# Kernel tuning notes

Measured on AMD Instinct MI355X. Metric: run time of the kernel, lower is better.

The kernel has to match this reference:

```python
import jax, jax.numpy as jnp
import numpy as np

K = 128      # knowledge_n (= net1 = prednet output width)
LOW = 64     # low_dim
PP = 64      # pp_dim
STU = 50000  # student_n
EXER = 20000 # exer_n
S_RANGES = [(0, 9999), (10000, 19999)]
NR = len(S_RANGES)
B = 4096


def setup_inputs() -> dict:
    key = jax.random.key(0)
    ks = jax.random.split(key, 16)

    def xavier(k, shape):
        fan_in, fan_out = shape[-1], shape[-2] if len(shape) > 1 else shape[-1]
        lim = np.sqrt(6.0 / (fan_in + fan_out))
        return jax.random.uniform(k, shape, jnp.float32, -lim, lim)

    return {
        "stu_id": jax.random.randint(ks[0], (B,), 0, STU),
        "exer_id": jax.random.randint(ks[1], (B,), 0, EXER),
        "kn_emb": jnp.ones((B, K), jnp.float32),
        "student_emb": xavier(ks[2], (NR, STU, LOW)),          # ParameterList stacked
        "prompt_stu": xavier(ks[3], (STU, PP)),
        "knowledge_emb": jax.random.normal(ks[4], (K, LOW), jnp.float32),
        "k_difficulty": xavier(ks[5], (EXER, LOW)),
        "s_exer_vectors": jax.random.uniform(ks[6], (NR, PP), jnp.float32),
        "W1": xavier(ks[7], (K, K + LOW)),                      # prednet_full1 (no bias)
        "W2": xavier(ks[8], (K, K + LOW)),                      # prednet_full2 (no bias)
        "W3": xavier(ks[9], (1, K)),                            # prednet_full3
        "b3": jnp.zeros((1,), jnp.float32),
        "fc1_W": xavier(ks[10], (K, PP + K)),
        "fc1_b": jnp.zeros((K,), jnp.float32),
        "fc2_W": xavier(ks[11], (K, PP + K)),
        "fc2_b": jnp.zeros((K,), jnp.float32),
    }


def reference(stu_id, exer_id, kn_emb, student_emb, prompt_stu, knowledge_emb,
              k_difficulty, s_exer_vectors, W1, W2, W3, b3, fc1_W, fc1_b, fc2_W, fc2_b):
    sig = jax.nn.sigmoid
    kle = knowledge_emb  # [K, LOW]

    # --- student side ---
    # prompt_stu.repeat(NR, 1) then index_select == index prompt_stu with stu_id % STU
    p_stu = prompt_stu[stu_id % STU]                              # [B, PP]
    stu_cat = student_emb.reshape(NR * STU, LOW)                  # concat of ParameterList
    old_stu = sig(stu_cat[stu_id] @ kle.T)                        # [B, K]
    stu_e = sig(jnp.concatenate([p_stu, old_stu], 1) @ fc1_W.T + fc1_b)  # [B, K]

    # --- exercise side ---
    counts = np.array([r[1] - r[0] + 1 for r in S_RANGES])
    temp_vectors = jnp.repeat(s_exer_vectors, counts, axis=0, total_repeat_length=EXER)
    p_exer = sig(temp_vectors[exer_id])                           # [B, PP]
    old_exer = sig(sig(k_difficulty[exer_id]) @ kle.T)            # [B, K]
    exer_e = sig(jnp.concatenate([p_exer, old_exer], 1) @ fc2_W.T + fc2_b)  # [B, K]

    # --- per-concept interaction ---
    # cat([x_broadcast, kn_vector], 2) @ W.T splits into x @ Wa.T + kle @ Wb.T
    W1a, W1b = W1[:, :K], W1[:, K:]
    W2a, W2b = W2[:, :K], W2[:, K:]
    preference = sig((stu_e @ W1a.T)[:, None, :] + (kle @ W1b.T)[None, :, :])   # [B, K, K]
    diff = sig((exer_e @ W2a.T)[:, None, :] + (kle @ W2b.T)[None, :, :])        # [B, K, K]

    o = sig((preference - diff) @ W3.T + b3)                      # [B, K, 1]
    sum_out = jnp.sum(o * kn_emb[:, :, None], axis=1)             # [B, 1]
    count = jnp.sum(kn_emb, axis=1, keepdims=True)
    return sum_out / count
```

## Files before the change

kernel.cpp:

```cpp
#include <hip/hip_runtime.h>
#include <hip/hip_bf16.h>

#define STUN   50000
#define BATCH  4096
#define LOG2E  1.4426950408889634f

__device__ __forceinline__ float fexp2(float x){ return __builtin_amdgcn_exp2f(x); }
__device__ __forceinline__ float frcp (float x){ return __builtin_amdgcn_rcpf(x); }
__device__ __forceinline__ float fsig (float x){ return frcp(1.0f + fexp2(-LOG2E * x)); }

__global__ __launch_bounds__(128) void k_pre(
    const float* __restrict__ kle,
    const float* __restrict__ W1,
    const float* __restrict__ W2,
    const float* __restrict__ fc1_W,
    const float* __restrict__ fc2_W,
    float* __restrict__ kleT,
    float* __restrict__ fc1T,
    float* __restrict__ fc2T,
    float* __restrict__ W1aT,
    float* __restrict__ W2aT,
    float* __restrict__ E1i,
    float* __restrict__ E2i)
{
    const int bid = blockIdx.x;
    const int t   = threadIdx.x;
    if (bid < 64) {
        const int u = bid;
        kleT[u * 128 + t] = kle[t * 64 + u];
    } else if (bid < 256) {
        const int u = bid - 64;
        fc1T[u * 128 + t] = fc1_W[t * 192 + u];
    } else if (bid < 448) {
        const int u = bid - 256;
        fc2T[u * 128 + t] = fc2_W[t * 192 + u];
    } else if (bid < 576) {
        const int u = bid - 448;
        W1aT[u * 128 + t] = W1[t * 192 + u];
    } else if (bid < 704) {
        const int u = bid - 576;
        W2aT[u * 128 + t] = W2[t * 192 + u];
    } else if (bid < 832) {
        const int j = bid - 704;
        float acc = 0.f;
        #pragma unroll
        for (int u4 = 0; u4 < 16; ++u4) {
            const float4 kv = *(const float4*)&kle[t * 64 + u4 * 4];
            const float4 wv = *(const float4*)&W1[j * 192 + 128 + u4 * 4];
            acc += kv.x * wv.x + kv.y * wv.y + kv.z * wv.z + kv.w * wv.w;
        }
        E1i[((j >> 2) * 128 + t) * 4 + (j & 3)] = fexp2(-LOG2E * acc);
    } else {
        const int j = bid - 832;
        float acc = 0.f;
        #pragma unroll
        for (int u4 = 0; u4 < 16; ++u4) {
            const float4 kv = *(const float4*)&kle[t * 64 + u4 * 4];
            const float4 wv = *(const float4*)&W2[j * 192 + 128 + u4 * 4];
            acc += kv.x * wv.x + kv.y * wv.y + kv.z * wv.z + kv.w * wv.w;
        }
        E2i[((j >> 2) * 128 + t) * 4 + (j & 3)] = fexp2(-LOG2E * acc);
    }
}

__global__ __launch_bounds__(256, 2) void k_prep(
    const int*   __restrict__ stu_id,
    const int*   __restrict__ exer_id,
    const float* __restrict__ student_emb,
    const float* __restrict__ prompt_stu,
    const float* __restrict__ k_diff,
    const float* __restrict__ s_exer,
    const float* __restrict__ kleT,
    const float* __restrict__ fc1T,
    const float* __restrict__ fc2T,
    const float* __restrict__ W1aT,
    const float* __restrict__ W2aT,
    const float* __restrict__ fc1_b,
    const float* __restrict__ fc2_b,
    float* __restrict__ es1o,
    float* __restrict__ es2o)
{
    __shared__ __align__(16) float sh_in [4][64][8];
    __shared__ __align__(16) float sh_old[2][128][12];
    __shared__ __align__(16) float sh_e  [2][128][12];
    __shared__ __align__(16) float ps[4][2][32][36];

    const int t  = threadIdx.x;
    const int b0 = blockIdx.x * 8;

    {
        const int g   = t >> 5;
        const int l   = t & 31;
        const int sid = stu_id[b0 + g];
        const int eid = exer_id[b0 + g];
        const int er  = (eid >= 10000) ? 1 : 0;
        #pragma unroll
        for (int it = 0; it < 2; ++it) {
            const int u = l + 32 * it;
            sh_in[0][u][g] = student_emb[sid * 64 + u];
            sh_in[1][u][g] = fsig(k_diff[eid * 64 + u]);
            sh_in[2][u][g] = prompt_stu[(sid % STUN) * 64 + u];
            sh_in[3][u][g] = fsig(s_exer[er * 64 + u]);
        }
    }
    __syncthreads();

    const int wv   = t >> 6;
    const int l    = t & 63;
    const int half = l >> 5;
    const int iq   = l & 31;
    float* myps = &ps[wv][half][iq][0];

    const int ch   = t >> 7;
    const int cidx = t & 127;
    const int ciq  = cidx >> 2;
    const int cc   = cidx & 3;

    float a[4][8];

#define CLR { _Pragma("unroll") for (int c = 0; c < 4; ++c) \
              _Pragma("unroll") for (int b = 0; b < 8; ++b) a[c][b] = 0.f; }

#define FMAC(c, wc) { \
    a[c][0] = fmaf(wc, x0.x, a[c][0]); a[c][1] = fmaf(wc, x0.y, a[c][1]); \
    a[c][2] = fmaf(wc, x0.z, a[c][2]); a[c][3] = fmaf(wc, x0.w, a[c][3]); \
    a[c][4] = fmaf(wc, x1.x, a[c][4]); a[c][5] = fmaf(wc, x1.y, a[c][5]); \
    a[c][6] = fmaf(wc, x1.z, a[c][6]); a[c][7] = fmaf(wc, x1.w, a[c][7]); }

#define GSTEP(wp, xp) { \
    const float4 w4 = *(const float4*)(wp); \
    const float4 x0 = *(const float4*)&(xp)[0]; \
    const float4 x1 = *(const float4*)&(xp)[4]; \
    FMAC(0, w4.x); FMAC(1, w4.y); FMAC(2, w4.z); FMAC(3, w4.w); }

#define PSTORE { _Pragma("unroll") for (int b = 0; b < 8; ++b) \
    *(float4*)&myps[b * 4] = make_float4(a[0][b], a[1][b], a[2][b], a[3][b]); }

#define PCOMB(res) float res[8]; \
    _Pragma("unroll") for (int b = 0; b < 8; ++b) \
        res[b] = ps[0][ch][ciq][b * 4 + cc] + ps[1][ch][ciq][b * 4 + cc] \
               + ps[2][ch][ciq][b * 4 + cc] + ps[3][ch][ciq][b * 4 + cc];

    CLR;
    {
        const int u0 = wv * 16;
        #pragma unroll 4
        for (int u = u0; u < u0 + 16; ++u)
            GSTEP(&kleT[u * 128 + iq * 4], sh_in[half][u]);
    }
    PSTORE;
    __syncthreads();
    {
        PCOMB(s);
        #pragma unroll
        for (int b = 0; b < 8; ++b) sh_old[ch][cidx][b] = fsig(s[b]);
    }
    __syncthreads();

    CLR;
    {
        const float* fcT = half ? fc2T : fc1T;
        const int u0 = wv * 48;
        const int ue_in = (u0 + 48 < 64) ? u0 + 48 : 64;
        #pragma unroll 4
        for (int u = u0; u < ue_in; ++u)
            GSTEP(&fcT[u * 128 + iq * 4], sh_in[2 + half][u]);
        const int us_old = (u0 > 64) ? u0 : 64;
        #pragma unroll 4
        for (int u = us_old; u < u0 + 48; ++u)
            GSTEP(&fcT[u * 128 + iq * 4], sh_old[half][u - 64]);
    }
    PSTORE;
    __syncthreads();
    {
        PCOMB(s);
        const float bias = (ch ? fc2_b : fc1_b)[cidx];
        #pragma unroll
        for (int b = 0; b < 8; ++b) sh_e[ch][cidx][b] = fsig(s[b] + bias);
    }
    __syncthreads();

    CLR;
    {
        const float* WT = half ? W2aT : W1aT;
        const int u0 = wv * 32;
        #pragma unroll 4
        for (int u = u0; u < u0 + 32; ++u)
            GSTEP(&WT[u * 128 + iq * 4], sh_e[half][u]);
    }
    PSTORE;
    __syncthreads();
    {
        PCOMB(s);
        float* eso = ch ? es2o : es1o;
        #pragma unroll
        for (int b = 0; b < 8; ++b)
            eso[(b0 + b) * 128 + cidx] = fexp2(-LOG2E * s[b]);
    }
#undef CLR
#undef FMAC
#undef GSTEP
#undef PSTORE
#undef PCOMB
}

__global__ __launch_bounds__(256, 6) void k_main(
    const float* __restrict__ es1o,
    const float* __restrict__ es2o,
    const float* __restrict__ E1i,
    const float* __restrict__ E2i,
    const float* __restrict__ W3,
    const float* __restrict__ b3,
    const float* __restrict__ kn,
    float* __restrict__ out)
{
    __shared__ __align__(16) float ses[2][2][128];
    __shared__ float sW3[128];
    __shared__ __align__(16) float redj[2][64][2];
    __shared__ float red2_o[2][2];
    __shared__ float red2_k[2][2];

    const int t   = threadIdx.x;
    const int b0  = blockIdx.x * 2;

    if (t < 128) {
        const int row  = t >> 5;
        const int col4 = (t & 31) * 4;
        const float* src = (row < 2) ? es1o : es2o;
        *(float4*)&ses[row >> 1][row & 1][col4] =
            *(const float4*)&src[(b0 + (row & 1)) * 128 + col4];
    } else if (t < 160) {
        const int q = t - 128;
        *(float4*)&sW3[q * 4] = *(const float4*)&W3[q * 4];
    }
    __syncthreads();

    const int w   = t >> 6;
    const int kk  = t & 63;
    const int kh  = w & 1;
    const int jh  = w >> 1;
    const int k2  = kh * 64 + kk;

    const float4* E1v = (const float4*)E1i;
    const float4* E2v = (const float4*)E2i;

    float acc0 = 0.f, acc1 = 0.f;

#define COMP(acc, esv1, esv2, e1c, e2c, w3c) { \
        const float uu = (esv1) * (e1c); \
        const float vv = (esv2) * (e2c); \
        const float dd = frcp((1.f + uu) * (1.f + vv)); \
        acc += ((vv - uu) * dd) * (w3c); }

    #pragma unroll 4
    for (int j4 = 0; j4 < 16; ++j4) {
        const int jj4 = jh * 16 + j4;
        const int j   = jj4 * 4;
        const float4 e1  = E1v[jj4 * 128 + k2];
        const float4 e2  = E2v[jj4 * 128 + k2];
        const float4 w3  = *(const float4*)&sW3[j];
        const float4 s1a = *(const float4*)&ses[0][0][j];
        const float4 s1b = *(const float4*)&ses[0][1][j];
        const float4 s2a = *(const float4*)&ses[1][0][j];
        const float4 s2b = *(const float4*)&ses[1][1][j];

        COMP(acc0, s1a.x, s2a.x, e1.x, e2.x, w3.x);
        COMP(acc0, s1a.y, s2a.y, e1.y, e2.y, w3.y);
        COMP(acc0, s1a.z, s2a.z, e1.z, e2.z, w3.z);
        COMP(acc0, s1a.w, s2a.w, e1.w, e2.w, w3.w);
        COMP(acc1, s1b.x, s2b.x, e1.x, e2.x, w3.x);
        COMP(acc1, s1b.y, s2b.y, e1.y, e2.y, w3.y);
        COMP(acc1, s1b.z, s2b.z, e1.z, e2.z, w3.z);
        COMP(acc1, s1b.w, s2b.w, e1.w, e2.w, w3.w);
    }
#undef COMP

    if (jh == 1) {
        redj[kh][kk][0] = acc0;
        redj[kh][kk][1] = acc1;
    }
    __syncthreads();
    if (jh == 0) {
        const float bb3 = b3[0];
        const float t0 = acc0 + redj[kh][kk][0];
        const float t1 = acc1 + redj[kh][kk][1];
        const float o0 = fsig(t0 + bb3);
        const float o1 = fsig(t1 + bb3);
        const float kn0 = kn[(b0 + 0) * 128 + k2];
        const float kn1 = kn[(b0 + 1) * 128 + k2];
        float co0 = o0 * kn0, ck0 = kn0;
        float co1 = o1 * kn1, ck1 = kn1;
        #pragma unroll
        for (int off = 1; off < 64; off <<= 1) {
            co0 += __shfl_xor(co0, off);
            ck0 += __shfl_xor(ck0, off);
            co1 += __shfl_xor(co1, off);
            ck1 += __shfl_xor(ck1, off);
        }
        if (kk == 0) {
            red2_o[kh][0] = co0; red2_o[kh][1] = co1;
            red2_k[kh][0] = ck0; red2_k[kh][1] = ck1;
        }
    }
    __syncthreads();
    if (t < 2) {
        const float so = red2_o[0][t] + red2_o[1][t];
        const float sk = red2_k[0][t] + red2_k[1][t];
        out[b0 + t] = so / sk;
    }
}

extern "C" void kernel_launch(void* const* d_in, const int* in_sizes, int n_in,
                              void* d_out, int out_size, void* d_ws, size_t ws_size,
                              hipStream_t stream)
{
    const int*   stu_id      = (const int*)  d_in[0];
    const int*   exer_id     = (const int*)  d_in[1];
    const float* kn_emb      = (const float*)d_in[2];
    const float* student_emb = (const float*)d_in[3];
    const float* prompt_stu  = (const float*)d_in[4];
    const float* kle         = (const float*)d_in[5];
    const float* k_diff      = (const float*)d_in[6];
    const float* s_exer      = (const float*)d_in[7];
    const float* W1          = (const float*)d_in[8];
    const float* W2          = (const float*)d_in[9];
    const float* W3          = (const float*)d_in[10];
    const float* b3          = (const float*)d_in[11];
    const float* fc1_W       = (const float*)d_in[12];
    const float* fc1_b       = (const float*)d_in[13];
    const float* fc2_W       = (const float*)d_in[14];
    const float* fc2_b       = (const float*)d_in[15];
    float* out = (float*)d_out;

    float* ws   = (float*)d_ws;
    float* kleT = ws;
    float* fc1T = kleT + 8192;
    float* fc2T = fc1T + 24576;
    float* W1aT = fc2T + 24576;
    float* W2aT = W1aT + 16384;
    float* E1i  = W2aT + 16384;
    float* E2i  = E1i  + 16384;
    float* es1o = E2i  + 16384;
    float* es2o = es1o + BATCH * 128;

    k_pre <<<960, 128, 0, stream>>>(kle, W1, W2, fc1_W, fc2_W,
                                    kleT, fc1T, fc2T, W1aT, W2aT, E1i, E2i);
    k_prep<<<BATCH / 8, 256, 0, stream>>>(stu_id, exer_id, student_emb, prompt_stu,
                                          k_diff, s_exer, kleT, fc1T, fc2T,
                                          W1aT, W2aT, fc1_b, fc2_b, es1o, es2o);
    k_main<<<BATCH / 2, 256, 0, stream>>>(es1o, es2o, E1i, E2i, W3, b3, kn_emb, out);
}
```

Baseline: 48.03 us.

## Fuse per-sample prep and pairwise interaction kernels into one launch

Merges k_prep and k_main into a single kernel that processes 4 samples per block. The per-sample es1/es2 exponentials stay in shared memory instead of round-tripping through global memory, and one kernel launch is removed. Each block now also walks all 128 j values per k, so the cross-wave j reduction goes away. The cost is halving the batch per block in the GEMM phase, which means more reloads of the weight matrices per sample, and the pairwise phase loses the 2-way j split.

```diff
diff --git a/kernel.cpp b/kernel.cpp
--- a/kernel.cpp
+++ b/kernel.cpp
@@ -63,7 +63,7 @@
     }
 }
 
-__global__ __launch_bounds__(256, 2) void k_prep(
+__global__ __launch_bounds__(256, 4) void k_fused(
     const int*   __restrict__ stu_id,
     const int*   __restrict__ exer_id,
     const float* __restrict__ student_emb,
@@ -77,31 +77,34 @@
     const float* __restrict__ W2aT,
     const float* __restrict__ fc1_b,
     const float* __restrict__ fc2_b,
-    float* __restrict__ es1o,
-    float* __restrict__ es2o)
+    const float* __restrict__ E1i,
+    const float* __restrict__ E2i,
+    const float* __restrict__ W3,
+    const float* __restrict__ b3,
+    const float* __restrict__ kn,
+    float* __restrict__ out)
 {
-    __shared__ __align__(16) float sh_in [4][64][8];
-    __shared__ __align__(16) float sh_old[2][128][12];
-    __shared__ __align__(16) float sh_e  [2][128][12];
-    __shared__ __align__(16) float ps[4][2][32][36];
+    __shared__ __align__(16) float sh_in [4][64][4];
+    __shared__ __align__(16) float sh_old[2][128][4];
+    __shared__ __align__(16) float sh_e  [2][128][4];
+    __shared__ __align__(16) float ps[4][2][32][20];
+    __shared__ __align__(16) float ses[2][4][128];
+    __shared__ float r_o[4][2];
+    __shared__ float r_k[4][2];
 
     const int t  = threadIdx.x;
-    const int b0 = blockIdx.x * 8;
-
-    {
-        const int g   = t >> 5;
-        const int l   = t & 31;
+    const int b0 = blockIdx.x * 4;
+
+    {
+        const int g   = t >> 6;
+        const int u   = t & 63;
         const int sid = stu_id[b0 + g];
         const int eid = exer_id[b0 + g];
         const int er  = (eid >= 10000) ? 1 : 0;
-        #pragma unroll
-        for (int it = 0; it < 2; ++it) {
-            const int u = l + 32 * it;
-            sh_in[0][u][g] = student_emb[sid * 64 + u];
-            sh_in[1][u][g] = fsig(k_diff[eid * 64 + u]);
-            sh_in[2][u][g] = prompt_stu[(sid % STUN) * 64 + u];
-            sh_in[3][u][g] = fsig(s_exer[er * 64 + u]);
-        }
+        sh_in[0][u][g] = student_emb[sid * 64 + u];
+        sh_in[1][u][g] = fsig(k_diff[eid * 64 + u]);
+        sh_in[2][u][g] = prompt_stu[(sid % STUN) * 64 + u];
+        sh_in[3][u][g] = fsig(s_exer[er * 64 + u]);
     }
     __syncthreads();
 
@@ -116,28 +119,25 @@
     const int ciq  = cidx >> 2;
     const int cc   = cidx & 3;
 
-    float a[4][8];
+    float a[4][4];
 
 #define CLR { _Pragma("unroll") for (int c = 0; c < 4; ++c) \
-              _Pragma("unroll") for (int b = 0; b < 8; ++b) a[c][b] = 0.f; }
+              _Pragma("unroll") for (int b = 0; b < 4; ++b) a[c][b] = 0.f; }
 
 #define FMAC(c, wc) { \
     a[c][0] = fmaf(wc, x0.x, a[c][0]); a[c][1] = fmaf(wc, x0.y, a[c][1]); \
-    a[c][2] = fmaf(wc, x0.z, a[c][2]); a[c][3] = fmaf(wc, x0.w, a[c][3]); \
-    a[c][4] = fmaf(wc, x1.x, a[c][4]); a[c][5] = fmaf(wc, x1.y, a[c][5]); \
-    a[c][6] = fmaf(wc, x1.z, a[c][6]); a[c][7] = fmaf(wc, x1.w, a[c][7]); }
+    a[c][2] = fmaf(wc, x0.z, a[c][2]); a[c][3] = fmaf(wc, x0.w, a[c][3]); }
 
 #define GSTEP(wp, xp) { \
     const float4 w4 = *(const float4*)(wp); \
     const float4 x0 = *(const float4*)&(xp)[0]; \
-    const float4 x1 = *(const float4*)&(xp)[4]; \
     FMAC(0, w4.x); FMAC(1, w4.y); FMAC(2, w4.z); FMAC(3, w4.w); }
 
-#define PSTORE { _Pragma("unroll") for (int b = 0; b < 8; ++b) \
+#define PSTORE { _Pragma("unroll") for (int b = 0; b < 4; ++b) \
     *(float4*)&myps[b * 4] = make_float4(a[0][b], a[1][b], a[2][b], a[3][b]); }
 
-#define PCOMB(res) float res[8]; \
-    _Pragma("unroll") for (int b = 0; b < 8; ++b) \
+#define PCOMB(res) float res[4]; \
+    _Pragma("unroll") for (int b = 0; b < 4; ++b) \
         res[b] = ps[0][ch][ciq][b * 4 + cc] + ps[1][ch][ciq][b * 4 + cc] \
                + ps[2][ch][ciq][b * 4 + cc] + ps[3][ch][ciq][b * 4 + cc];
 
@@ -153,7 +153,7 @@
     {
         PCOMB(s);
         #pragma unroll
-        for (int b = 0; b < 8; ++b) sh_old[ch][cidx][b] = fsig(s[b]);
+        for (int b = 0; b < 4; ++b) sh_old[ch][cidx][b] = fsig(s[b]);
     }
     __syncthreads();
 
@@ -176,7 +176,7 @@
         PCOMB(s);
         const float bias = (ch ? fc2_b : fc1_b)[cidx];
         #pragma unroll
-        for (int b = 0; b < 8; ++b) sh_e[ch][cidx][b] = fsig(s[b] + bias);
+        for (int b = 0; b < 4; ++b) sh_e[ch][cidx][b] = fsig(s[b] + bias);
     }
     __syncthreads();
 
@@ -192,57 +192,23 @@
     __syncthreads();
     {
         PCOMB(s);
-        float* eso = ch ? es2o : es1o;
-        #pragma unroll
-        for (int b = 0; b < 8; ++b)
-            eso[(b0 + b) * 128 + cidx] = fexp2(-LOG2E * s[b]);
+        #pragma unroll
+        for (int b = 0; b < 4; ++b)
+            ses[ch][b][cidx] = fexp2(-LOG2E * s[b]);
     }
 #undef CLR
 #undef FMAC
 #undef GSTEP
 #undef PSTORE
 #undef PCOMB
-}
-
-__global__ __launch_bounds__(256, 6) void k_main(
-    const float* __restrict__ es1o,
-    const float* __restrict__ es2o,
-    const float* __restrict__ E1i,
-    const float* __restrict__ E2i,
-    const float* __restrict__ W3,
-    const float* __restrict__ b3,
-    const float* __restrict__ kn,
-    float* __restrict__ out)
-{
-    __shared__ __align__(16) float ses[2][2][128];
-    __shared__ float sW3[128];
-    __shared__ __align__(16) float redj[2][64][2];
-    __shared__ float red2_o[2][2];
-    __shared__ float red2_k[2][2];
-
-    const int t   = threadIdx.x;
-    const int b0  = blockIdx.x * 2;
-
-    if (t < 128) {
-        const int row  = t >> 5;
-        const int col4 = (t & 31) * 4;
-        const float* src = (row < 2) ? es1o : es2o;
-        *(float4*)&ses[row >> 1][row & 1][col4] =
-            *(const float4*)&src[(b0 + (row & 1)) * 128 + col4];
-    } else if (t < 160) {
-        const int q = t - 128;
-        *(float4*)&sW3[q * 4] = *(const float4*)&W3[q * 4];
-    }
-    __syncthreads();
-
-    const int w   = t >> 6;
-    const int kk  = t & 63;
-    const int kh  = w & 1;
-    const int jh  = w >> 1;
-    const int k2  = kh * 64 + kk;
-
-    const float4* E1v = (const float4*)E1i;
-    const float4* E2v = (const float4*)E2i;
+    __syncthreads();
+
+    const int k  = t & 127;
+    const int bh = t >> 7;
+    const int i0 = bh * 2;
+
+    const float4* E1v = (const float4*)E1i + k;
+    const float4* E2v = (const float4*)E2i + k;
 
     float acc0 = 0.f, acc1 = 0.f;
 
@@ -250,63 +216,55 @@
         const float uu = (esv1) * (e1c); \
         const float vv = (esv2) * (e2c); \
         const float dd = frcp((1.f + uu) * (1.f + vv)); \
-        acc += ((vv - uu) * dd) * (w3c); }
+        acc = fmaf((vv - uu) * dd, (w3c), acc); }
 
     #pragma unroll 4
-    for (int j4 = 0; j4 < 16; ++j4) {
-        const int jj4 = jh * 16 + j4;
-        const int j   = jj4 * 4;
-        const float4 e1  = E1v[jj4 * 128 + k2];
-        const float4 e2  = E2v[jj4 * 128 + k2];
-        const float4 w3  = *(const float4*)&sW3[j];
-        const float4 s1a = *(const float4*)&ses[0][0][j];
-        const float4 s1b = *(const float4*)&ses[0][1][j];
-        const float4 s2a = *(const float4*)&ses[1][0][j];
-        const float4 s2b = *(const float4*)&ses[1][1][j];
-
-        COMP(acc0, s1a.x, s2a.x, e1.x, e2.x, w3.x);
-        COMP(acc0, s1a.y, s2a.y, e1.y, e2.y, w3.y);
-        COMP(acc0, s1a.z, s2a.z, e1.z, e2.z, w3.z);
-        COMP(acc0, s1a.w, s2a.w, e1.w, e2.w, w3.w);
-        COMP(acc1, s1b.x, s2b.x, e1.x, e2.x, w3.x);
-        COMP(acc1, s1b.y, s2b.y, e1.y, e2.y, w3.y);
-        COMP(acc1, s1b.z, s2b.z, e1.z, e2.z, w3.z);
-        COMP(acc1, s1b.w, s2b.w, e1.w, e2.w, w3.w);
+    for (int j4 = 0; j4 < 32; ++j4) {
+        const int j = j4 * 4;
+        const float4 e1  = E1v[j4 * 128];
+        const float4 e2  = E2v[j4 * 128];
+        const float4 w3  = *(const float4*)&W3[j];
+        const float4 p1a = *(const float4*)&ses[0][i0 + 0][j];
+        const float4 p2a = *(const float4*)&ses[1][i0 + 0][j];
+        const float4 p1b = *(const float4*)&ses[0][i0 + 1][j];
+        const float4 p2b = *(const float4*)&ses[1][i0 + 1][j];
+        COMP(acc0, p1a.x, p2a.x, e1.x, e2.x, w3.x);
+        COMP(acc0, p1a.y, p2a.y, e1.y, e2.y, w3.y);
+        COMP(acc0, p1a.z, p2a.z, e1.z, e2.z, w3.z);
+        COMP(acc0, p1a.w, p2a.w, e1.w, e2.w, w3.w);
+        COMP(acc1, p1b.x, p2b.x, e1.x, e2.x, w3.x);
+        COMP(acc1, p1b.y, p2b.y, e1.y, e2.y, w3.y);
+        COMP(acc1, p1b.z, p2b.z, e1.z, e2.z, w3.z);
+        COMP(acc1, p1b.w, p2b.w, e1.w, e2.w, w3.w);
     }
 #undef COMP
 
-    if (jh == 1) {
-        redj[kh][kk][0] = acc0;
-        redj[kh][kk][1] = acc1;
-    }
-    __syncthreads();
-    if (jh == 0) {
-        const float bb3 = b3[0];
-        const float t0 = acc0 + redj[kh][kk][0];
-        const float t1 = acc1 + redj[kh][kk][1];
-        const float o0 = fsig(t0 + bb3);
-        const float o1 = fsig(t1 + bb3);
-        const float kn0 = kn[(b0 + 0) * 128 + k2];
-        const float kn1 = kn[(b0 + 1) * 128 + k2];
-        float co0 = o0 * kn0, ck0 = kn0;
-        float co1 = o1 * kn1, ck1 = kn1;
-        #pragma unroll
-        for (int off = 1; off < 64; off <<= 1) {
-            co0 += __shfl_xor(co0, off);
-            ck0 += __shfl_xor(ck0, off);
-            co1 += __shfl_xor(co1, off);
-            ck1 += __shfl_xor(ck1, off);
-        }
-        if (kk == 0) {
-            red2_o[kh][0] = co0; red2_o[kh][1] = co1;
-            red2_k[kh][0] = ck0; red2_k[kh][1] = ck1;
-        }
-    }
-    __syncthreads();
-    if (t < 2) {
-        const float so = red2_o[0][t] + red2_o[1][t];
-        const float sk = red2_k[0][t] + red2_k[1][t];
-        out[b0 + t] = so / sk;
+    const float bb3 = b3[0];
+    const float o0  = fsig(acc0 + bb3);
+    const float o1  = fsig(acc1 + bb3);
+    const float kn0 = kn[(b0 + i0 + 0) * 128 + k];
+    const float kn1 = kn[(b0 + i0 + 1) * 128 + k];
+    float co0 = o0 * kn0, ck0 = kn0;
+    float co1 = o1 * kn1, ck1 = kn1;
+    #pragma unroll
+    for (int off = 1; off < 64; off <<= 1) {
+        co0 += __shfl_xor(co0, off);
+        ck0 += __shfl_xor(ck0, off);
+        co1 += __shfl_xor(co1, off);
+        ck1 += __shfl_xor(ck1, off);
+    }
+    const int w = t >> 6;
+    if ((t & 63) == 0) {
+        r_o[w][0] = co0; r_o[w][1] = co1;
+        r_k[w][0] = ck0; r_k[w][1] = ck1;
+    }
+    __syncthreads();
+    if (t < 4) {
+        const int bhh = t >> 1;
+        const int i   = t & 1;
+        const float so = r_o[bhh * 2][i] + r_o[bhh * 2 + 1][i];
+        const float sk = r_k[bhh * 2][i] + r_k[bhh * 2 + 1][i];
+        out[b0 + bhh * 2 + i] = so / sk;
     }
 }
 
@@ -340,13 +298,11 @@
     float* W2aT = W1aT + 16384;
     float* E1i  = W2aT + 16384;
     float* E2i  = E1i  + 16384;
-    float* es1o = E2i  + 16384;
-    float* es2o = es1o + BATCH * 128;
-
-    k_pre <<<960, 128, 0, stream>>>(kle, W1, W2, fc1_W, fc2_W,
-                                    kleT, fc1T, fc2T, W1aT, W2aT, E1i, E2i);
-    k_prep<<<BATCH / 8, 256, 0, stream>>>(stu_id, exer_id, student_emb, prompt_stu,
-                                          k_diff, s_exer, kleT, fc1T, fc2T,
-                                          W1aT, W2aT, fc1_b, fc2_b, es1o, es2o);
-    k_main<<<BATCH / 2, 256, 0, stream>>>(es1o, es2o, E1i, E2i, W3, b3, kn_emb, out);
+
+    k_pre  <<<960, 128, 0, stream>>>(kle, W1, W2, fc1_W, fc2_W,
+                                     kleT, fc1T, fc2T, W1aT, W2aT, E1i, E2i);
+    k_fused<<<BATCH / 4, 256, 0, stream>>>(stu_id, exer_id, student_emb, prompt_stu,
+                                           k_diff, s_exer, kleT, fc1T, fc2T,
+                                           W1aT, W2aT, fc1_b, fc2_b,
+                                           E1i, E2i, W3, b3, kn_emb, out);
 }
```

After: 46.41 us, median of 2. 1.03x faster.
